# Kernel optimization log

Hardware: AMD Instinct MI355X
Metric: run time of the kernel (lower is better)

The kernel has to match this reference:

```python
import jax, jax.numpy as jnp
import numpy as np

NUM_ELEC = 128
TIME_STEPS = 128  # must equal NUM_ELEC for the original module's matmuls to be shape-consistent
NUM_VOXELS = 2052
HIDDEN = 64
DCT_DIM = 512
BATCH = 64
RHO = 0.5
TAU = 0.1
PLV_THRESH = 0.5


def dct_matrix(N, K):
    n = np.arange(N)[None, :]
    k = np.arange(K)[:, None]
    m = np.sqrt(2.0 / N) * np.cos(np.pi * (2 * n + 1) * k / (2 * N))
    m[0, :] = 1.0 / np.sqrt(N)
    return jnp.asarray(m, dtype=jnp.float32)


def setup_inputs() -> dict:
    ks = jax.random.split(jax.random.key(0), 12)
    H = HIDDEN
    return {
        "z": jax.random.normal(ks[0], (BATCH, NUM_ELEC, TIME_STEPS), dtype=jnp.float32),
        "lead_field": jax.random.normal(ks[1], (NUM_VOXELS, NUM_ELEC), dtype=jnp.float32),
        "gumbel_u": jax.random.uniform(ks[2], (NUM_ELEC, NUM_ELEC), dtype=jnp.float32, minval=1e-6, maxval=1.0 - 1e-6),
        "w_gae": jax.random.normal(ks[3], (NUM_ELEC, H), dtype=jnp.float32) / np.sqrt(NUM_ELEC),
        "b_gae": jnp.zeros((H,), dtype=jnp.float32),
        "w1": jax.random.normal(ks[4], (NUM_ELEC, H), dtype=jnp.float32) / np.sqrt(NUM_ELEC),
        "b1": jnp.zeros((H,), dtype=jnp.float32),
        "w2": jax.random.normal(ks[5], (H, H), dtype=jnp.float32) / np.sqrt(H),
        "b2": jnp.zeros((H,), dtype=jnp.float32),
        "w_ih": jax.random.normal(ks[6], (3 * H, H), dtype=jnp.float32) / np.sqrt(H),
        "w_hh": jax.random.normal(ks[7], (3 * H, H), dtype=jnp.float32) / np.sqrt(H),
        "b_ih": jnp.zeros((3 * H,), dtype=jnp.float32),
        "b_hh": jnp.zeros((3 * H,), dtype=jnp.float32),
    }


def _hilbert_phases(z):
    # FFT-based analytic signal along last axis (== scipy.signal.hilbert), then instantaneous phase
    T = z.shape[-1]
    idx = jnp.arange(T)
    hf = jnp.where(idx == 0, 1.0, jnp.where(idx < T // 2, 2.0, jnp.where(idx == T // 2, 1.0, 0.0)))
    analytic = jnp.fft.ifft(jnp.fft.fft(z, axis=-1) * hf, axis=-1)
    return jnp.angle(analytic)


def _forward(z, lead_field, gumbel_u, w_gae, b_gae, w1, b1, w2, b2, w_ih, w_hh, b_ih, b_hh):
    B, N, T = z.shape
    # ---- PLV adjacency: fused broadcast+reduction replacing the 128x128 python double loop ----
    phases = _hilbert_phases(z)                                  # [B,N,T]
    E = jnp.exp(1j * phases).astype(jnp.complex64)
    # plv[i,j] = |mean_{b,t} exp(i(phi_i - phi_j))| = |E_i . conj(E_j)| / (B*T)
    plv = jnp.abs(jnp.einsum('bit,bjt->ij', E, jnp.conj(E))) / (B * T)
    a = (plv >= PLV_THRESH).astype(jnp.float32)                  # [N,N]
    # ---- GAE: GCN encoder on batch-averaged signals + inner-product decoder ----
    x = jnp.mean(z, axis=0)                                      # [N,T] (T == N)
    hg = jax.nn.relu((a @ x) @ w_gae + b_gae)                    # [N,H]
    p = jax.nn.sigmoid(hg @ hg.T)                                # [N,N]
    # ---- Gumbel graph augmentation ----
    e = RHO * p + (1.0 - RHO) * a
    g = -jnp.log(-jnp.log(gumbel_u))
    a_aug = jax.nn.sigmoid((jnp.log(e) - jnp.log(1.0 - e) + g) / TAU)
    # ---- symmetric degree normalization ----
    d_inv_sqrt = jnp.sum(a_aug, axis=-1) ** -0.5
    a_norm = d_inv_sqrt[:, None] * a_aug * d_inv_sqrt[None, :]
    zT = jnp.swapaxes(z, 1, 2)                                   # [B,T,N]
    h = jax.nn.relu(jnp.matmul(a_norm, zT) @ w1 + b1)            # [B,N,H]
    h = jax.nn.relu(jnp.matmul(a_norm, h) @ w2 + b2)             # [B,N,H]
    h_seq = h.reshape(B * T, -1)                                 # [B*T,H]
    # ---- GRU over flattened (B*T) sequence (torch nn.GRU gate order r,z,n) ----
    Hd = w_hh.shape[1]
    def gru_step(hprev, xt):
        gi = xt @ w_ih.T + b_ih
        gh = hprev @ w_hh.T + b_hh
        ir, iz, inn = jnp.split(gi, 3)
        hr, hz, hn = jnp.split(gh, 3)
        r = jax.nn.sigmoid(ir + hr)
        zg = jax.nn.sigmoid(iz + hz)
        cand = jnp.tanh(inn + r * hn)
        hnew = (1.0 - zg) * cand + zg * hprev
        return hnew, hnew
    _, h_gru = jax.lax.scan(gru_step, jnp.zeros((Hd,), z.dtype), h_seq)
    del h_gru  # computed as in the original forward, but not part of the returned tuple
    # ---- lead-field projection + DCT low-pass reconstruction ----
    dct_m = dct_matrix(NUM_VOXELS, DCT_DIM)                      # [K,V]
    s = jnp.matmul(lead_field, zT)                               # [B,V,T]
    s_dct = jnp.matmul(dct_m, s)                                 # [B,K,T]
    s_low = s_dct[:, :DCT_DIM, :]                                # [B,K,T] (full, K == dct_dim)
    s_recon = jnp.matmul(dct_m.T, s_low)                         # [B,V,T]
    return s_low, s_recon, a_aug


def reference(z, lead_field, gumbel_u, w_gae, b_gae, w1, b1, w2, b2, w_ih, w_hh, b_ih, b_hh):
    return _forward(z, lead_field, gumbel_u, w_gae, b_gae, w1, b1, w2, b2, w_ih, w_hh, b_ih, b_hh)
```

## Files before the change

kernel.cpp:

```cpp
#include <hip/hip_runtime.h>

#define NV 2052
#define KD 512
#define RTOT 2564
#define KTOT 256
#define JTOT 8192

typedef __attribute__((ext_vector_type(8))) short short8v;
typedef __attribute__((ext_vector_type(4))) float f32x4;
typedef unsigned short ushort_t;

#define OFF_AF   0u
#define OFF_ABF  65536u
#define OFF_BBF  409600u
#define OFF_YBF  1458176u
#define OFF_PG   2506752u
#define OFF_PM1  6701056u
#define OFF_A    7749632u
#define OFF_X    7766016u
#define OFF_XW   7782400u

#define SREC_OFF 4194304u
#define AAUG_OFF 21004288u

#define GLOAD16(g, l) __builtin_amdgcn_global_load_lds( \
    (const __attribute__((address_space(1))) unsigned int*)(g), \
    (__attribute__((address_space(3))) unsigned int*)(l), 16, 0, 0)

__device__ __forceinline__ float dct_val(int k, int v) {
    if (k == 0) return 1.0f / sqrtf(2052.0f);
    int m = (2 * v + 1) * k;
    int r = m % 8208;
    float ang = (float)((double)r * (3.14159265358979323846 / 4104.0));
    return sqrtf(2.0f / 2052.0f) * cosf(ang);
}

__device__ __forceinline__ void bf16split(float x, ushort_t& hi, ushort_t& lo) {
    unsigned xb = __float_as_uint(x);
    hi = (ushort_t)(xb >> 16);
    float r = x - __uint_as_float((unsigned)hi << 16);
    lo = (ushort_t)(__float_as_uint(r) >> 16);
}

__device__ __forceinline__ ushort_t bf16rn(float x) {
    unsigned xb = __float_as_uint(x);
    return (ushort_t)((xb + 0x7fffu + ((xb >> 16) & 1u)) >> 16);
}

__global__ __launch_bounds__(256) void k_front(const float* __restrict__ LF, const float* __restrict__ z,
                                               float* __restrict__ Pm1,
                                               ushort_t* __restrict__ Ybf, ushort_t* __restrict__ Bbf) {
    __shared__ float sh[8][132];
    const int tid = threadIdx.x;
    const int bid = blockIdx.x;
    if (bid < 1024) {
        const int t = tid & 127;
        const int kk = tid >> 7;
        const int k0 = (bid & 63) * 8;
        const int vch = bid >> 6;
        const int v0 = vch * 128;
        const int nv = (vch == 15) ? 132 : 128;
        for (int p = tid; p < 1056; p += 256) {
            int rr = p / 132, cc = p - rr * 132;
            sh[rr][cc] = dct_val(k0 + rr, v0 + cc);
        }
        __syncthreads();
        const float* lf = LF + (size_t)v0 * 128 + t;
        float a0 = 0.f, a1 = 0.f, a2 = 0.f, a3 = 0.f;
        for (int vi = 0; vi + 2 <= nv; vi += 2) {
            float l0 = lf[vi * 128], l1 = lf[vi * 128 + 128];
            a0 += sh[kk + 0][vi] * l0; a1 += sh[kk + 2][vi] * l0;
            a2 += sh[kk + 4][vi] * l0; a3 += sh[kk + 6][vi] * l0;
            a0 += sh[kk + 0][vi + 1] * l1; a1 += sh[kk + 2][vi + 1] * l1;
            a2 += sh[kk + 4][vi + 1] * l1; a3 += sh[kk + 6][vi + 1] * l1;
        }
        float* P = Pm1 + (size_t)vch * 65536;
        P[(k0 + kk + 0) * 128 + t] = a0;
        P[(k0 + kk + 2) * 128 + t] = a1;
        P[(k0 + kk + 4) * 128 + t] = a2;
        P[(k0 + kk + 6) * 128 + t] = a3;
    } else {
        const int t = tid & 127;
        const int rr = tid >> 7;
        const int rid = (bid - 1024) * 2 + rr;
        const int b = rid >> 7, i = rid & 127;
        sh[rr][t] = z[(size_t)rid * 128 + t];
        if (tid < 128) {
            float hv = 0.f;
            if (t & 1) {
                float ang = 3.14159265358979323846f * (float)t * (1.0f / 128.0f);
                hv = (cosf(ang) / sinf(ang)) * (1.0f / 64.0f);
            }
            sh[2][t] = hv;
        }
        __syncthreads();
        float acc = 0.f;
        #pragma unroll 8
        for (int q = 0; q < 64; ++q) {
            int d = 2 * q + 1;
            acc += sh[2][d] * sh[rr][(t - d) & 127];
        }
        float zv = sh[rr][t];
        float inv = rsqrtf(zv * zv + acc * acc);
        Ybf[(size_t)i * JTOT + b * 128 + t] = bf16rn(zv * inv);
        Ybf[(size_t)(128 + i) * JTOT + b * 128 + t] = bf16rn(acc * inv);
        Bbf[(size_t)rid * 128 + t] = (ushort_t)(__float_as_uint(zv) >> 16);
    }
}

__global__ __launch_bounds__(256) void k_m1red(const float* __restrict__ Pm1, const float* __restrict__ z,
                                               float* __restrict__ AF, ushort_t* __restrict__ Abf,
                                               float* __restrict__ X) {
    const int bid = blockIdx.x;
    if (bid < 256) {
        int id = bid * 256 + threadIdx.x;
        float s = 0.f;
        #pragma unroll
        for (int p = 0; p < 16; ++p) s += Pm1[p * 65536 + id];
        AF[id] = s;
        int rid = id >> 7, t = id & 127;
        ushort_t hi, lo; bf16split(s, hi, lo);
        ushort_t* row = Abf + (size_t)rid * KTOT;
        row[t] = hi; row[128 + t] = lo;
    } else {
        int id = (bid - 256) * 256 + threadIdx.x;
        float s0 = 0.f, s1 = 0.f, s2 = 0.f, s3 = 0.f;
        #pragma unroll 4
        for (int b = 0; b < 64; b += 4) {
            s0 += z[(size_t)(b + 0) * 16384 + id];
            s1 += z[(size_t)(b + 1) * 16384 + id];
            s2 += z[(size_t)(b + 2) * 16384 + id];
            s3 += z[(size_t)(b + 3) * 16384 + id];
        }
        X[id] = ((s0 + s1) + (s2 + s3)) * (1.0f / 64.0f);
    }
}

__global__ __launch_bounds__(256) void k_m2(const float* __restrict__ M1, ushort_t* __restrict__ Abf) {
    __shared__ float sM1[128][128];
    __shared__ float sdct[8][128];
    const int tid = threadIdx.x;
    const int t = tid & 127;
    const int half = tid >> 7;
    const int v0 = blockIdx.x * 8;
    float acc0 = 0.f, acc1 = 0.f, acc2 = 0.f, acc3 = 0.f;
    for (int kc = 0; kc < KD; kc += 128) {
        __syncthreads();
        #pragma unroll
        for (int q = 0; q < 16; ++q) {
            int f = q * 256 + tid;
            int kr = f >> 5;
            int c4 = (f & 31) * 4;
            *(float4*)&sM1[kr][c4] = *(const float4*)&M1[(size_t)(kc + kr) * 128 + c4];
        }
        #pragma unroll
        for (int p = tid; p < 1024; p += 256)
            sdct[p >> 7][p & 127] = dct_val(kc + (p & 127), v0 + (p >> 7));
        __syncthreads();
        const float* d0 = &sdct[half * 4 + 0][0];
        const float* d1 = &sdct[half * 4 + 1][0];
        const float* d2 = &sdct[half * 4 + 2][0];
        const float* d3 = &sdct[half * 4 + 3][0];
        #pragma unroll 4
        for (int ki = 0; ki < 128; ++ki) {
            float m = sM1[ki][t];
            acc0 += d0[ki] * m;
            acc1 += d1[ki] * m;
            acc2 += d2[ki] * m;
            acc3 += d3[ki] * m;
        }
    }
    float vals[4] = {acc0, acc1, acc2, acc3};
    #pragma unroll
    for (int r = 0; r < 4; ++r) {
        int v = v0 + half * 4 + r;
        if (v < NV) {
            ushort_t hi, lo; bf16split(vals[r], hi, lo);
            ushort_t* row = Abf + (size_t)(KD + v) * KTOT;
            row[t] = hi; row[128 + t] = lo;
        }
    }
}

__global__ __launch_bounds__(256) void k_back(const ushort_t* __restrict__ Abf, const ushort_t* __restrict__ Bbf,
                                              const ushort_t* __restrict__ Ybf,
                                              float* __restrict__ out, float* __restrict__ Pg) {
    __shared__ ushort_t SM[24576];
    const int tid = threadIdx.x;
    const int wave = tid >> 6;
    const int lane = tid & 63;
    const int wr = wave >> 1, wc = wave & 1;
    const int l15 = lane & 15;
    const int lhi = lane >> 4;
    const int bid = blockIdx.x;

    f32x4 acc[4][4];
    #pragma unroll
    for (int i = 0; i < 4; ++i)
        #pragma unroll
        for (int j = 0; j < 4; ++j)
            acc[i][j] = (f32x4){0.f, 0.f, 0.f, 0.f};

    if (bid < 1344) {
        const int j0 = (bid & 63) * 128;
        const int r0 = (bid >> 6) * 128;
        ushort_t* AlHi = SM;
        ushort_t* AlLo = SM + 8192;
        ushort_t* Bl   = SM + 16384;
        for (int kc = 0; kc < 128; kc += 64) {
            __syncthreads();
            #pragma unroll
            for (int i = 0; i < 4; ++i) {
                int elt = (wave * 4 + i) * 64 + lane;
                int m = elt >> 3;
                int sc = (elt & 7) ^ (m & 7);
                GLOAD16(Abf + (size_t)(r0 + m) * KTOT + kc + sc * 8,       &AlHi[(wave * 4 + i) * 512]);
                GLOAD16(Abf + (size_t)(r0 + m) * KTOT + 128 + kc + sc * 8, &AlLo[(wave * 4 + i) * 512]);
                GLOAD16(Bbf + (size_t)(j0 + m) * 128 + kc + sc * 8,        &Bl[(wave * 4 + i) * 512]);
            }
            asm volatile("s_waitcnt vmcnt(0)" ::: "memory");
            __syncthreads();
            #pragma unroll
            for (int kk = 0; kk < 2; ++kk) {
                short8v ah[4], al[4], bv[4];
                #pragma unroll
                for (int mi = 0; mi < 4; ++mi) {
                    int m = wr * 64 + mi * 16 + l15;
                    int ch = (kk * 4 + lhi) ^ (m & 7);
                    ah[mi] = *(const short8v*)&AlHi[m * 64 + ch * 8];
                    al[mi] = *(const short8v*)&AlLo[m * 64 + ch * 8];
                }
                #pragma unroll
                for (int ni = 0; ni < 4; ++ni) {
                    int n = wc * 64 + ni * 16 + l15;
                    int ch = (kk * 4 + lhi) ^ (n & 7);
                    bv[ni] = *(const short8v*)&Bl[n * 64 + ch * 8];
                }
                #pragma unroll
                for (int mi = 0; mi < 4; ++mi)
                    #pragma unroll
                    for (int ni = 0; ni < 4; ++ni)
                        acc[mi][ni] = __builtin_amdgcn_mfma_f32_16x16x32_bf16(ah[mi], bv[ni], acc[mi][ni], 0, 0, 0);
                #pragma unroll
                for (int mi = 0; mi < 4; ++mi)
                    #pragma unroll
                    for (int ni = 0; ni < 4; ++ni)
                        acc[mi][ni] = __builtin_amdgcn_mfma_f32_16x16x32_bf16(al[mi], bv[ni], acc[mi][ni], 0, 0, 0);
            }
        }
        float* SMf = (float*)SM;
        const unsigned bb = (unsigned)(bid & 63);
        #pragma unroll
        for (int hhalf = 0; hhalf < 2; ++hhalf) {
            __syncthreads();
            if (wc == hhalf) {
                #pragma unroll
                for (int mi = 0; mi < 4; ++mi)
                    #pragma unroll
                    for (int ni = 0; ni < 4; ++ni)
                        #pragma unroll
                        for (int reg = 0; reg < 4; ++reg) {
                            int rl = wr * 64 + mi * 16 + lhi * 4 + reg;
                            int cl = ni * 16 + l15;
                            SMf[rl * 68 + cl] = acc[mi][ni][reg];
                        }
            }
            __syncthreads();
            int rl = tid >> 1;
            int cs = (tid & 1) * 32;
            int r = r0 + rl;
            if (r < RTOT) {
                unsigned base;
                if (r < KD) base = bb * 65536u + (unsigned)r * 128u;
                else        base = SREC_OFF + bb * 262656u + (unsigned)(r - KD) * 128u;
                base += hhalf * 64 + cs;
                const float* src = &SMf[rl * 68 + cs];
                float* dst = out + base;
                #pragma unroll
                for (int q = 0; q < 8; ++q)
                    *(float4*)(dst + q * 4) = *(const float4*)(src + q * 4);
            }
        }
    } else {
        const int g = bid - 1344;
        const int j0 = (g & 1) * 128;
        const int i0 = ((g >> 1) & 1) * 128;
        const int sk = g >> 2;
        const int kc0 = sk * 256;
        ushort_t* Al = SM;
        ushort_t* Bl = SM + 8192;
        for (int kc = kc0; kc < kc0 + 256; kc += 64) {
            __syncthreads();
            #pragma unroll
            for (int i = 0; i < 4; ++i) {
                int elt = (wave * 4 + i) * 64 + lane;
                int m = elt >> 3;
                int sc = (elt & 7) ^ (m & 7);
                GLOAD16(Ybf + (size_t)(i0 + m) * JTOT + kc + sc * 8, &Al[(wave * 4 + i) * 512]);
                GLOAD16(Ybf + (size_t)(j0 + m) * JTOT + kc + sc * 8, &Bl[(wave * 4 + i) * 512]);
            }
            asm volatile("s_waitcnt vmcnt(0)" ::: "memory");
            __syncthreads();
            #pragma unroll
            for (int kk = 0; kk < 2; ++kk) {
                short8v av[4], bv[4];
                #pragma unroll
                for (int mi = 0; mi < 4; ++mi) {
                    int m = wr * 64 + mi * 16 + l15;
                    int ch = (kk * 4 + lhi) ^ (m & 7);
                    av[mi] = *(const short8v*)&Al[m * 64 + ch * 8];
                }
                #pragma unroll
                for (int ni = 0; ni < 4; ++ni) {
                    int n = wc * 64 + ni * 16 + l15;
                    int ch = (kk * 4 + lhi) ^ (n & 7);
                    bv[ni] = *(const short8v*)&Bl[n * 64 + ch * 8];
                }
                #pragma unroll
                for (int mi = 0; mi < 4; ++mi)
                    #pragma unroll
                    for (int ni = 0; ni < 4; ++ni)
                        acc[mi][ni] = __builtin_amdgcn_mfma_f32_16x16x32_bf16(av[mi], bv[ni], acc[mi][ni], 0, 0, 0);
            }
        }
        const int q = ((g >> 1) & 1) * 2 + (g & 1);
        float* P = Pg + (size_t)(sk * 4 + q) * 16384;
        #pragma unroll
        for (int mi = 0; mi < 4; ++mi)
            #pragma unroll
            for (int reg = 0; reg < 4; ++reg) {
                int rl = wr * 64 + mi * 16 + lhi * 4 + reg;
                #pragma unroll
                for (int ni = 0; ni < 4; ++ni) {
                    int cl = wc * 64 + ni * 16 + l15;
                    P[rl * 128 + cl] = acc[mi][ni][reg];
                }
            }
    }
}

__global__ __launch_bounds__(256) void k_plvx(const float* __restrict__ Pg, const float* __restrict__ X,
                                              const float* __restrict__ Wg,
                                              float* __restrict__ A, float* __restrict__ XW) {
    const int bid = blockIdx.x;
    if (bid < 64) {
        int id = bid * 256 + threadIdx.x;
        float R = 0.f, I = 0.f;
        #pragma unroll 8
        for (int sk = 0; sk < 32; ++sk) {
            const float* P = Pg + (size_t)sk * 65536 + id;
            R += P[0] + P[3 * 16384];
            I += P[2 * 16384] - P[1 * 16384];
        }
        float plv = sqrtf(R * R + I * I) * (1.0f / 8192.0f);
        A[id] = (plv >= 0.5f) ? 1.0f : 0.0f;
    } else {
        int id = (bid - 64) * 256 + threadIdx.x;
        int e = id >> 6, h = id & 63;
        const float* xrow = X + (size_t)e * 128;
        float s = 0.f;
        #pragma unroll 4
        for (int t = 0; t < 128; ++t) s += xrow[t] * Wg[t * 64 + h];
        XW[id] = s;
    }
}

__global__ __launch_bounds__(256) void k_aaugf(const float* __restrict__ A, const float* __restrict__ XW,
                                               const float* __restrict__ bg, const float* __restrict__ U,
                                               float* __restrict__ out) {
    __shared__ float sXW[128][64];
    __shared__ float sHGT[64][128];
    const int tid = threadIdx.x;
    for (int p = tid; p < 8192; p += 256) sXW[p >> 6][p & 63] = XW[p];
    __syncthreads();
    {
        const int r = tid & 127;
        const int half = tid >> 7;
        const float* arow = A + (size_t)r * 128;
        float hacc[32];
        #pragma unroll
        for (int h = 0; h < 32; ++h) hacc[h] = 0.f;
        for (int j = 0; j < 128; ++j) {
            float av = arow[j];
            #pragma unroll
            for (int h = 0; h < 32; ++h) hacc[h] += av * sXW[j][half * 32 + h];
        }
        #pragma unroll
        for (int h = 0; h < 32; ++h)
            sHGT[half * 32 + h][r] = fmaxf(hacc[h] + bg[half * 32 + h], 0.f);
    }
    __syncthreads();
    const int id = blockIdx.x * 256 + tid;
    const int i = id >> 7, j = id & 127;
    float dot = 0.f;
    #pragma unroll 8
    for (int h = 0; h < 64; ++h) dot += sHGT[h][i] * sHGT[h][j];
    float p = 1.f / (1.f + expf(-dot));
    float e = 0.5f * p + 0.5f * A[id];
    float gmb = -logf(-logf(U[id]));
    float arg = (logf(e) - logf(1.f - e) + gmb) * 10.0f;
    out[AAUG_OFF + id] = 1.f / (1.f + expf(-arg));
}

extern "C" void kernel_launch(void* const* d_in, const int* in_sizes, int n_in,
                              void* d_out, int out_size, void* d_ws, size_t ws_size,
                              hipStream_t stream) {
    const float* z  = (const float*)d_in[0];
    const float* LF = (const float*)d_in[1];
    const float* U  = (const float*)d_in[2];
    const float* Wg = (const float*)d_in[3];
    const float* bg = (const float*)d_in[4];
    float* out = (float*)d_out;
    float* W = (float*)d_ws;

    float* AF  = W + OFF_AF;
    ushort_t* Abf = (ushort_t*)(W + OFF_ABF);
    ushort_t* Bbf = (ushort_t*)(W + OFF_BBF);
    ushort_t* Ybf = (ushort_t*)(W + OFF_YBF);
    float* Pg  = W + OFF_PG;
    float* Pm1 = W + OFF_PM1;
    float* A   = W + OFF_A;
    float* X   = W + OFF_X;
    float* XW  = W + OFF_XW;

    k_front<<<5120, 256, 0, stream>>>(LF, z, Pm1, Ybf, Bbf);
    k_m1red<<<320, 256, 0, stream>>>(Pm1, z, AF, Abf, X);
    k_m2   <<<257, 256, 0, stream>>>(AF, Abf);
    k_back <<<1472, 256, 0, stream>>>(Abf, Bbf, Ybf, out, Pg);
    k_plvx <<<96, 256, 0, stream>>>(Pg, X, Wg, A, XW);
    k_aaugf<<<64, 256, 0, stream>>>(A, XW, bg, U, out);
}
```

Measured before the change: 112.8 us.

## Move PLV Gram GEMM into k_m2 and fold PLV/XW reduction into k_back

The 128 blocks computing the PLV phase Gram partials move from k_back into k_m2, where they run alongside the small DCT projection blocks. The PLV reduction and X·W blocks from k_plvx become extra blocks at the end of k_back, which removes one kernel launch. The intent is to fill the under-occupied k_m2 grid and cut a launch boundary. In exchange, k_m2 blocks now have mixed workloads, and the fused tail blocks in k_back depend on Pg having been written by the previous kernel.

Measured after the change: 108.7 us. -3.6%, faster.

```diff
diff --git a/kernel.cpp b/kernel.cpp
--- a/kernel.cpp
+++ b/kernel.cpp
@@ -136,72 +136,142 @@
     }
 }
 
-__global__ __launch_bounds__(256) void k_m2(const float* __restrict__ M1, ushort_t* __restrict__ Abf) {
+__global__ __launch_bounds__(256) void k_m2(const float* __restrict__ M1, ushort_t* __restrict__ Abf,
+                                            const ushort_t* __restrict__ Ybf, float* __restrict__ Pg) {
     __shared__ float sM1[128][128];
     __shared__ float sdct[8][128];
     const int tid = threadIdx.x;
-    const int t = tid & 127;
-    const int half = tid >> 7;
-    const int v0 = blockIdx.x * 8;
-    float acc0 = 0.f, acc1 = 0.f, acc2 = 0.f, acc3 = 0.f;
-    for (int kc = 0; kc < KD; kc += 128) {
-        __syncthreads();
-        #pragma unroll
-        for (int q = 0; q < 16; ++q) {
-            int f = q * 256 + tid;
-            int kr = f >> 5;
-            int c4 = (f & 31) * 4;
-            *(float4*)&sM1[kr][c4] = *(const float4*)&M1[(size_t)(kc + kr) * 128 + c4];
-        }
-        #pragma unroll
-        for (int p = tid; p < 1024; p += 256)
-            sdct[p >> 7][p & 127] = dct_val(kc + (p & 127), v0 + (p >> 7));
-        __syncthreads();
-        const float* d0 = &sdct[half * 4 + 0][0];
-        const float* d1 = &sdct[half * 4 + 1][0];
-        const float* d2 = &sdct[half * 4 + 2][0];
-        const float* d3 = &sdct[half * 4 + 3][0];
-        #pragma unroll 4
-        for (int ki = 0; ki < 128; ++ki) {
-            float m = sM1[ki][t];
-            acc0 += d0[ki] * m;
-            acc1 += d1[ki] * m;
-            acc2 += d2[ki] * m;
-            acc3 += d3[ki] * m;
-        }
+    const int bid = blockIdx.x;
+    if (bid < 257) {
+        const int t = tid & 127;
+        const int half = tid >> 7;
+        const int v0 = bid * 8;
+        float acc0 = 0.f, acc1 = 0.f, acc2 = 0.f, acc3 = 0.f;
+        for (int kc = 0; kc < KD; kc += 128) {
+            __syncthreads();
+            #pragma unroll
+            for (int q = 0; q < 16; ++q) {
+                int f = q * 256 + tid;
+                int kr = f >> 5;
+                int c4 = (f & 31) * 4;
+                *(float4*)&sM1[kr][c4] = *(const float4*)&M1[(size_t)(kc + kr) * 128 + c4];
+            }
+            #pragma unroll
+            for (int p = tid; p < 1024; p += 256)
+                sdct[p >> 7][p & 127] = dct_val(kc + (p & 127), v0 + (p >> 7));
+            __syncthreads();
+            const float* d0 = &sdct[half * 4 + 0][0];
+            const float* d1 = &sdct[half * 4 + 1][0];
+            const float* d2 = &sdct[half * 4 + 2][0];
+            const float* d3 = &sdct[half * 4 + 3][0];
+            #pragma unroll 4
+            for (int ki = 0; ki < 128; ++ki) {
+                float m = sM1[ki][t];
+                acc0 += d0[ki] * m;
+                acc1 += d1[ki] * m;
+                acc2 += d2[ki] * m;
+                acc3 += d3[ki] * m;
+            }
+        }
+        float vals[4] = {acc0, acc1, acc2, acc3};
+        #pragma unroll
+        for (int r = 0; r < 4; ++r) {
+            int v = v0 + half * 4 + r;
+            if (v < NV) {
+                ushort_t hi, lo; bf16split(vals[r], hi, lo);
+                ushort_t* row = Abf + (size_t)(KD + v) * KTOT;
+                row[t] = hi; row[128 + t] = lo;
+            }
+        }
+    } else {
+        const int g = bid - 257;
+        const int j0 = (g & 1) * 128;
+        const int i0 = ((g >> 1) & 1) * 128;
+        const int sk = g >> 2;
+        const int kc0 = sk * 256;
+        const int wave = tid >> 6;
+        const int lane = tid & 63;
+        const int wr = wave >> 1, wc = wave & 1;
+        const int l15 = lane & 15;
+        const int lhi = lane >> 4;
+        ushort_t* Al = (ushort_t*)&sM1[0][0];
+        ushort_t* Bl = Al + 8192;
+        f32x4 acc[4][4];
+        #pragma unroll
+        for (int i = 0; i < 4; ++i)
+            #pragma unroll
+            for (int j = 0; j < 4; ++j)
+                acc[i][j] = (f32x4){0.f, 0.f, 0.f, 0.f};
+        for (int kc = kc0; kc < kc0 + 256; kc += 64) {
+            __syncthreads();
+            #pragma unroll
+            for (int i = 0; i < 4; ++i) {
+                int elt = (wave * 4 + i) * 64 + lane;
+                int m = elt >> 3;
+                int sc = (elt & 7) ^ (m & 7);
+                GLOAD16(Ybf + (size_t)(i0 + m) * JTOT + kc + sc * 8, &Al[(wave * 4 + i) * 512]);
+                GLOAD16(Ybf + (size_t)(j0 + m) * JTOT + kc + sc * 8, &Bl[(wave * 4 + i) * 512]);
+            }
+            asm volatile("s_waitcnt vmcnt(0)" ::: "memory");
+            __syncthreads();
+            #pragma unroll
+            for (int kk = 0; kk < 2; ++kk) {
+                short8v av[4], bv[4];
+                #pragma unroll
+                for (int mi = 0; mi < 4; ++mi) {
+                    int m = wr * 64 + mi * 16 + l15;
+                    int ch = (kk * 4 + lhi) ^ (m & 7);
+                    av[mi] = *(const short8v*)&Al[m * 64 + ch * 8];
+                }
+                #pragma unroll
+                for (int ni = 0; ni < 4; ++ni) {
+                    int n = wc * 64 + ni * 16 + l15;
+                    int ch = (kk * 4 + lhi) ^ (n & 7);
+                    bv[ni] = *(const short8v*)&Bl[n * 64 + ch * 8];
+                }
+                #pragma unroll
+                for (int mi = 0; mi < 4; ++mi)
+                    #pragma unroll
+                    for (int ni = 0; ni < 4; ++ni)
+                        acc[mi][ni] = __builtin_amdgcn_mfma_f32_16x16x32_bf16(av[mi], bv[ni], acc[mi][ni], 0, 0, 0);
+            }
+        }
+        const int q = ((g >> 1) & 1) * 2 + (g & 1);
+        float* P = Pg + (size_t)(sk * 4 + q) * 16384;
+        #pragma unroll
+        for (int mi = 0; mi < 4; ++mi)
+            #pragma unroll
+            for (int reg = 0; reg < 4; ++reg) {
+                int rl = wr * 64 + mi * 16 + lhi * 4 + reg;
+                #pragma unroll
+                for (int ni = 0; ni < 4; ++ni) {
+                    int cl = wc * 64 + ni * 16 + l15;
+                    P[rl * 128 + cl] = acc[mi][ni][reg];
+                }
+            }
     }
-    float vals[4] = {acc0, acc1, acc2, acc3};
-    #pragma unroll
-    for (int r = 0; r < 4; ++r) {
-        int v = v0 + half * 4 + r;
-        if (v < NV) {
-            ushort_t hi, lo; bf16split(vals[r], hi, lo);
-            ushort_t* row = Abf + (size_t)(KD + v) * KTOT;
-            row[t] = hi; row[128 + t] = lo;
-        }
-    }
 }
 
 __global__ __launch_bounds__(256) void k_back(const ushort_t* __restrict__ Abf, const ushort_t* __restrict__ Bbf,
-                                              const ushort_t* __restrict__ Ybf,
-                                              float* __restrict__ out, float* __restrict__ Pg) {
+                                              float* __restrict__ out, const float* __restrict__ Pg,
+                                              const float* __restrict__ X, const float* __restrict__ Wg,
+                                              float* __restrict__ A, float* __restrict__ XW) {
     __shared__ ushort_t SM[24576];
     const int tid = threadIdx.x;
-    const int wave = tid >> 6;
-    const int lane = tid & 63;
-    const int wr = wave >> 1, wc = wave & 1;
-    const int l15 = lane & 15;
-    const int lhi = lane >> 4;
     const int bid = blockIdx.x;
 
-    f32x4 acc[4][4];
-    #pragma unroll
-    for (int i = 0; i < 4; ++i)
-        #pragma unroll
-        for (int j = 0; j < 4; ++j)
-            acc[i][j] = (f32x4){0.f, 0.f, 0.f, 0.f};
-
     if (bid < 1344) {
+        const int wave = tid >> 6;
+        const int lane = tid & 63;
+        const int wr = wave >> 1, wc = wave & 1;
+        const int l15 = lane & 15;
+        const int lhi = lane >> 4;
+        f32x4 acc[4][4];
+        #pragma unroll
+        for (int i = 0; i < 4; ++i)
+            #pragma unroll
+            for (int j = 0; j < 4; ++j)
+                acc[i][j] = (f32x4){0.f, 0.f, 0.f, 0.f};
         const int j0 = (bid & 63) * 128;
         const int r0 = (bid >> 6) * 128;
         ushort_t* AlHi = SM;
@@ -281,70 +351,8 @@
                     *(float4*)(dst + q * 4) = *(const float4*)(src + q * 4);
             }
         }
-    } else {
-        const int g = bid - 1344;
-        const int j0 = (g & 1) * 128;
-        const int i0 = ((g >> 1) & 1) * 128;
-        const int sk = g >> 2;
-        const int kc0 = sk * 256;
-        ushort_t* Al = SM;
-        ushort_t* Bl = SM + 8192;
-        for (int kc = kc0; kc < kc0 + 256; kc += 64) {
-            __syncthreads();
-            #pragma unroll
-            for (int i = 0; i < 4; ++i) {
-                int elt = (wave * 4 + i) * 64 + lane;
-                int m = elt >> 3;
-                int sc = (elt & 7) ^ (m & 7);
-                GLOAD16(Ybf + (size_t)(i0 + m) * JTOT + kc + sc * 8, &Al[(wave * 4 + i) * 512]);
-                GLOAD16(Ybf + (size_t)(j0 + m) * JTOT + kc + sc * 8, &Bl[(wave * 4 + i) * 512]);
-            }
-            asm volatile("s_waitcnt vmcnt(0)" ::: "memory");
-            __syncthreads();
-            #pragma unroll
-            for (int kk = 0; kk < 2; ++kk) {
-                short8v av[4], bv[4];
-                #pragma unroll
-                for (int mi = 0; mi < 4; ++mi) {
-                    int m = wr * 64 + mi * 16 + l15;
-                    int ch = (kk * 4 + lhi) ^ (m & 7);
-                    av[mi] = *(const short8v*)&Al[m * 64 + ch * 8];
-                }
-                #pragma unroll
-                for (int ni = 0; ni < 4; ++ni) {
-                    int n = wc * 64 + ni * 16 + l15;
-                    int ch = (kk * 4 + lhi) ^ (n & 7);
-                    bv[ni] = *(const short8v*)&Bl[n * 64 + ch * 8];
-                }
-                #pragma unroll
-                for (int mi = 0; mi < 4; ++mi)
-                    #pragma unroll
-                    for (int ni = 0; ni < 4; ++ni)
-                        acc[mi][ni] = __builtin_amdgcn_mfma_f32_16x16x32_bf16(av[mi], bv[ni], acc[mi][ni], 0, 0, 0);
-            }
-        }
-        const int q = ((g >> 1) & 1) * 2 + (g & 1);
-        float* P = Pg + (size_t)(sk * 4 + q) * 16384;
-        #pragma unroll
-        for (int mi = 0; mi < 4; ++mi)
-            #pragma unroll
-            for (int reg = 0; reg < 4; ++reg) {
-                int rl = wr * 64 + mi * 16 + lhi * 4 + reg;
-                #pragma unroll
-                for (int ni = 0; ni < 4; ++ni) {
-                    int cl = wc * 64 + ni * 16 + l15;
-                    P[rl * 128 + cl] = acc[mi][ni][reg];
-                }
-            }
-    }
-}
-
-__global__ __launch_bounds__(256) void k_plvx(const float* __restrict__ Pg, const float* __restrict__ X,
-                                              const float* __restrict__ Wg,
-                                              float* __restrict__ A, float* __restrict__ XW) {
-    const int bid = blockIdx.x;
-    if (bid < 64) {
-        int id = bid * 256 + threadIdx.x;
+    } else if (bid < 1408) {
+        int id = (bid - 1344) * 256 + tid;
         float R = 0.f, I = 0.f;
         #pragma unroll 8
         for (int sk = 0; sk < 32; ++sk) {
@@ -355,7 +363,7 @@
         float plv = sqrtf(R * R + I * I) * (1.0f / 8192.0f);
         A[id] = (plv >= 0.5f) ? 1.0f : 0.0f;
     } else {
-        int id = (bid - 64) * 256 + threadIdx.x;
+        int id = (bid - 1408) * 256 + tid;
         int e = id >> 6, h = id & 63;
         const float* xrow = X + (size_t)e * 128;
         float s = 0.f;
@@ -425,8 +433,7 @@
 
     k_front<<<5120, 256, 0, stream>>>(LF, z, Pm1, Ybf, Bbf);
     k_m1red<<<320, 256, 0, stream>>>(Pm1, z, AF, Abf, X);
-    k_m2   <<<257, 256, 0, stream>>>(AF, Abf);
-    k_back <<<1472, 256, 0, stream>>>(Abf, Bbf, Ybf, out, Pg);
-    k_plvx <<<96, 256, 0, stream>>>(Pg, X, Wg, A, XW);
+    k_m2   <<<385, 256, 0, stream>>>(AF, Abf, Ybf, Pg);
+    k_back <<<1440, 256, 0, stream>>>(Abf, Bbf, out, Pg, X, Wg, A, XW);
     k_aaugf<<<64, 256, 0, stream>>>(A, XW, bg, U, out);
 }
```
